# Performance work log

Measured on AMD Instinct MI355X. Metric: run time of the kernel, lower is better.

## Reference

```python
import jax, jax.numpy as jnp
import numpy as np
from jax import lax

L, D, H, F, T = 4, 512, 8, 2048, 1000
B, S = 8, 1024

def setup_inputs() -> dict:
    key = jax.random.key(0)
    ks = jax.random.split(key, 12)
    s = 0.02
    return {
        'features': jax.random.normal(ks[0], (B, S, D), jnp.float32),
        'Wq': jax.random.normal(ks[1], (L, D, D), jnp.float32) * s,
        'Wk': jax.random.normal(ks[2], (L, D, D), jnp.float32) * s,
        'Wv': jax.random.normal(ks[3], (L, D, D), jnp.float32) * s,
        'bq': jnp.zeros((L, D), jnp.float32),
        'bk': jnp.zeros((L, D), jnp.float32),
        'bv': jnp.zeros((L, D), jnp.float32),
        'Wo': jax.random.normal(ks[4], (L, D, D), jnp.float32) * s,
        'bo': jnp.zeros((L, D), jnp.float32),
        'ln1_g': jnp.ones((L, D), jnp.float32),
        'ln1_b': jnp.zeros((L, D), jnp.float32),
        'ln2_g': jnp.ones((L, D), jnp.float32),
        'ln2_b': jnp.zeros((L, D), jnp.float32),
        'W1': jax.random.normal(ks[5], (L, F, D), jnp.float32) * s,
        'b1': jnp.zeros((L, F), jnp.float32),
        'W2': jax.random.normal(ks[6], (L, D, F), jnp.float32) * s,
        'b2': jnp.zeros((L, D), jnp.float32),
        'Wout': jax.random.normal(ks[7], (D, D), jnp.float32) * s,
        'bout': jnp.zeros((D,), jnp.float32),
    }

def _layernorm(x, g, b, eps=1e-5):
    mu = jnp.mean(x, axis=-1, keepdims=True)
    var = jnp.var(x, axis=-1, keepdims=True)
    return (x - mu) / jnp.sqrt(var + eps) * g + b

def _ddim_noise(features):
    betas = jnp.linspace(1e-4, 0.02, T)
    alphas_cumprod = jnp.cumprod(1.0 - betas)
    base = jax.random.key(42)
    def step(x, t):
        a = alphas_cumprod[t]
        noise = jax.random.normal(jax.random.fold_in(base, t), x.shape, x.dtype)
        return jnp.sqrt(a) * x + jnp.sqrt(1.0 - a) * noise, None
    x, _ = lax.scan(step, features, jnp.arange(1, T))
    return x

def reference(features, Wq, Wk, Wv, bq, bk, bv, Wo, bo, ln1_g, ln1_b, ln2_g, ln2_b, W1, b1, W2, b2, Wout, bout):
    x = _ddim_noise(features)  # [B,S,D]
    dh = D // H
    scale = 1.0 / jnp.sqrt(jnp.float32(dh))
    for l in range(L):
        # multi-head self-attention (post-norm, no dropout at eval)
        q = (x @ Wq[l].T + bq[l]).reshape(B, S, H, dh).transpose(0, 2, 1, 3)
        k = (x @ Wk[l].T + bk[l]).reshape(B, S, H, dh).transpose(0, 2, 1, 3)
        v = (x @ Wv[l].T + bv[l]).reshape(B, S, H, dh).transpose(0, 2, 1, 3)
        scores = jnp.einsum('bhqd,bhkd->bhqk', q, k) * scale
        attn = jax.nn.softmax(scores, axis=-1)
        o = jnp.einsum('bhqk,bhkd->bhqd', attn, v).transpose(0, 2, 1, 3).reshape(B, S, D)
        o = o @ Wo[l].T + bo[l]
        x = _layernorm(x + o, ln1_g[l], ln1_b[l])
        # feed-forward (ReLU, PyTorch default)
        ff = jax.nn.relu(x @ W1[l].T + b1[l]) @ W2[l].T + b2[l]
        x = _layernorm(x + ff, ln2_g[l], ln2_b[l])
    return x @ Wout.T + bout
```

## Files before the change

### kernel.cpp

```cpp
#include <hip/hip_runtime.h>
#include <stdint.h>
#include <math.h>

typedef unsigned short u16;
typedef __bf16 bf16x8 __attribute__((ext_vector_type(8)));
typedef float f32x4 __attribute__((ext_vector_type(4)));
typedef short s16x8 __attribute__((ext_vector_type(8)));
union B8 { s16x8 s; bf16x8 b; };

__device__ __forceinline__ u16 f2bf(float f) {
    union { __bf16 h; u16 u; } r;
    r.h = (__bf16)f;
    return r.u;
}
__device__ __forceinline__ uint32_t pk2bf(float a, float b) {
    union { __bf16 h[2]; uint32_t u; } r;
    r.h[0] = (__bf16)a; r.h[1] = (__bf16)b;
    return r.u;
}
__device__ __forceinline__ float bf2f(u16 u) {
    return __uint_as_float(((uint32_t)u) << 16);
}
__device__ __forceinline__ float fexp2(float x) {
    return __builtin_amdgcn_exp2f(x);
}

typedef const __attribute__((address_space(1))) uint32_t* gas_t;
typedef __attribute__((address_space(3))) uint32_t* las_t;
__device__ __forceinline__ void gld16(const void* g, void* l) {
    __builtin_amdgcn_global_load_lds((gas_t)g, (las_t)l, 16, 0, 0);
}

__host__ __forceinline__ uint32_t rotl32(uint32_t x, int d) {
    return (x << d) | (x >> (32 - d));
}
__device__ __forceinline__ uint32_t rotl_d(uint32_t x, int d) {
    return __builtin_amdgcn_alignbit(x, x, (uint32_t)(32 - d));
}

__host__ inline void tf2x32_h(uint32_t k0, uint32_t k1, uint32_t& x0, uint32_t& x1) {
    uint32_t k2 = k0 ^ k1 ^ 0x1BD11BDAu;
    x0 += k0; x1 += k1;
    x0 += x1; x1 = rotl32(x1, 13); x1 ^= x0;
    x0 += x1; x1 = rotl32(x1, 15); x1 ^= x0;
    x0 += x1; x1 = rotl32(x1, 26); x1 ^= x0;
    x0 += x1; x1 = rotl32(x1,  6); x1 ^= x0;
    x0 += k1; x1 += k2 + 1u;
    x0 += x1; x1 = rotl32(x1, 17); x1 ^= x0;
    x0 += x1; x1 = rotl32(x1, 29); x1 ^= x0;
    x0 += x1; x1 = rotl32(x1, 16); x1 ^= x0;
    x0 += x1; x1 = rotl32(x1, 24); x1 ^= x0;
    x0 += k2; x1 += k0 + 2u;
    x0 += x1; x1 = rotl32(x1, 13); x1 ^= x0;
    x0 += x1; x1 = rotl32(x1, 15); x1 ^= x0;
    x0 += x1; x1 = rotl32(x1, 26); x1 ^= x0;
    x0 += x1; x1 = rotl32(x1,  6); x1 ^= x0;
    x0 += k0; x1 += k1 + 3u;
    x0 += x1; x1 = rotl32(x1, 17); x1 ^= x0;
    x0 += x1; x1 = rotl32(x1, 29); x1 ^= x0;
    x0 += x1; x1 = rotl32(x1, 16); x1 ^= x0;
    x0 += x1; x1 = rotl32(x1, 24); x1 ^= x0;
    x0 += k1; x1 += k2 + 4u;
    x0 += x1; x1 = rotl32(x1, 13); x1 ^= x0;
    x0 += x1; x1 = rotl32(x1, 15); x1 ^= x0;
    x0 += x1; x1 = rotl32(x1, 26); x1 ^= x0;
    x0 += x1; x1 = rotl32(x1,  6); x1 ^= x0;
    x0 += k2; x1 += k0 + 5u;
}

__device__ __forceinline__ void tf2x32_d(uint32_t k0, uint32_t k1,
                                         uint32_t& x0, uint32_t& x1) {
    uint32_t k2 = k0 ^ k1 ^ 0x1BD11BDAu;
    x0 += k0; x1 += k1;
    x0 += x1; x1 = rotl_d(x1, 13); x1 ^= x0;
    x0 += x1; x1 = rotl_d(x1, 15); x1 ^= x0;
    x0 += x1; x1 = rotl_d(x1, 26); x1 ^= x0;
    x0 += x1; x1 = rotl_d(x1,  6); x1 ^= x0;
    x0 += k1; x1 += k2 + 1u;
    x0 += x1; x1 = rotl_d(x1, 17); x1 ^= x0;
    x0 += x1; x1 = rotl_d(x1, 29); x1 ^= x0;
    x0 += x1; x1 = rotl_d(x1, 16); x1 ^= x0;
    x0 += x1; x1 = rotl_d(x1, 24); x1 ^= x0;
    x0 += k2; x1 += k0 + 2u;
    x0 += x1; x1 = rotl_d(x1, 13); x1 ^= x0;
    x0 += x1; x1 = rotl_d(x1, 15); x1 ^= x0;
    x0 += x1; x1 = rotl_d(x1, 26); x1 ^= x0;
    x0 += x1; x1 = rotl_d(x1,  6); x1 ^= x0;
    x0 += k0; x1 += k1 + 3u;
    x0 += x1; x1 = rotl_d(x1, 17); x1 ^= x0;
    x0 += x1; x1 = rotl_d(x1, 29); x1 ^= x0;
    x0 += x1; x1 = rotl_d(x1, 16); x1 ^= x0;
    x0 += x1; x1 = rotl_d(x1, 24); x1 ^= x0;
    x0 += k1; x1 += k2 + 4u;
    x0 += x1; x1 = rotl_d(x1, 13); x1 ^= x0;
    x0 += x1; x1 = rotl_d(x1, 15); x1 ^= x0;
    x0 += x1; x1 = rotl_d(x1, 26); x1 ^= x0;
    x0 += x1; x1 = rotl_d(x1,  6); x1 ^= x0;
    x0 += k2; x1 += k0 + 5u;
}

__device__ __forceinline__ float erfinv_f(float x) {
    float w = -__logf(fmaf(x, -x, 1.0f));
    float p;
    if (w < 5.0f) {
        w = w - 2.5f;
        p = 2.81022636e-08f;
        p = p * w + 3.43273939e-07f;
        p = p * w + -3.5233877e-06f;
        p = p * w + -4.39150654e-06f;
        p = p * w + 0.00021858087f;
        p = p * w + -0.00125372503f;
        p = p * w + -0.00417768164f;
        p = p * w + 0.246640727f;
        p = p * w + 1.50140941f;
    } else {
        w = sqrtf(w) - 3.0f;
        p = -0.000200214257f;
        p = p * w + 0.000100950558f;
        p = p * w + 0.00134934322f;
        p = p * w + -0.00367342844f;
        p = p * w + 0.00573950773f;
        p = p * w + -0.0076224613f;
        p = p * w + 0.00943887047f;
        p = p * w + 1.00167406f;
        p = p * w + 2.83297682f;
    }
    return p * x;
}

__device__ __forceinline__ float tf_normal(uint32_t k0, uint32_t k1, uint32_t idx) {
    uint32_t x0 = 0u, x1 = idx;
    tf2x32_d(k0, k1, x0, x1);
    uint32_t bits = x0 ^ x1;
    float f = __uint_as_float((bits >> 9) | 0x3f800000u) - 1.0f;
    float u = f * 2.0f - 0.99999994f;
    u = fmaxf(-0.99999994f, u);
    return 1.41421354f * erfinv_f(u);
}

__global__ __launch_bounds__(256) void noise_kernel(
    u16* __restrict__ xb,
    uint32_t ka0, uint32_t ka1, float ca,
    uint32_t kb0, uint32_t kb1, float cb, int n4)
{
    int i = blockIdx.x * 256 + threadIdx.x;
    if (i >= n4) return;
    ushort4 vb;
    #pragma unroll
    for (int e = 0; e < 4; ++e) {
        uint32_t idx = (uint32_t)(i * 4 + e);
        float a = ca * tf_normal(ka0, ka1, idx)
                + cb * tf_normal(kb0, kb1, idx);
        (&vb.x)[e] = f2bf(a);
    }
    ((ushort4*)xb)[i] = vb;
}

__global__ __launch_bounds__(256) void cvt_all_kernel(
    const float* __restrict__ Wq, const float* __restrict__ Wk,
    const float* __restrict__ Wv, const float* __restrict__ Wo,
    const float* __restrict__ W1, const float* __restrict__ W2,
    const float* __restrict__ Wout, u16* __restrict__ dst, int n4)
{
    int i = blockIdx.x * 256 + threadIdx.x;
    if (i >= n4) return;
    int e = i * 4;
    const float* src;
    if (e < 3145728) {
        int l = e / 786432;
        int rem = e - l * 786432;
        int sel = rem >> 18;
        int off = rem & 262143;
        src = (sel == 0 ? Wq : sel == 1 ? Wk : Wv) + l * 262144 + off;
    } else if (e < 4194304) src = Wo + (e - 3145728);
    else if (e < 8388608)  src = W1 + (e - 4194304);
    else if (e < 12582912) src = W2 + (e - 8388608);
    else                   src = Wout + (e - 12582912);
    float4 v = *(const float4*)src;
    uint2 o;
    o.x = pk2bf(v.x, v.y);
    o.y = pk2bf(v.z, v.w);
    *(uint2*)(dst + e) = o;
}

template<int EPI>
__global__ __launch_bounds__(512) void gemm64u(
    const u16* __restrict__ A, const u16* __restrict__ Bw,
    const float* __restrict__ bias0, const float* __restrict__ bias1,
    const float* __restrict__ bias2, const u16* __restrict__ resid,
    void* __restrict__ out0, void* __restrict__ out1, void* __restrict__ out2,
    int N, int K)
{
    constexpr int ACH = 16;
    constexpr int ASZ = 128 * 64, BSZ = 64 * 64;
    __shared__ __align__(16) u16 At[2 * ASZ];
    __shared__ __align__(16) u16 Bt[2 * BSZ];
    const int tid = threadIdx.x;
    const int l = tid & 63;
    const int w = tid >> 6;
    const int wr = w >> 1, wc = w & 1;

    int lid = blockIdx.y * gridDim.x + blockIdx.x;
    int nwg = gridDim.x * gridDim.y;
    int nlid = (lid & 7) * (nwg >> 3) + (lid >> 3);
    int mb = nlid / gridDim.x;
    int nb = nlid - mb * gridDim.x;

    const int lrow = l >> 3;
    const int lch  = (l & 7) ^ lrow;

    const u16* aTile = A  + (size_t)(mb * 128) * K + (size_t)lrow * K + lch * 8;
    const u16* bTile = Bw + (size_t)(nb * 64) * K + (size_t)lrow * K + lch * 8;

    f32x4 acc[2][2] = {};

    auto stage = [&](int buf, int k0) {
        #pragma unroll
        for (int i = 0; i < 3; ++i) {
            int c = w * 3 + i;
            if (c < ACH) gld16(aTile + (size_t)(c * 8) * K + k0, &At[buf * ASZ + c * 512]);
            else gld16(bTile + (size_t)((c - ACH) * 8) * K + k0, &Bt[buf * BSZ + (c - ACH) * 512]);
        }
    };
    auto compute = [&](int buf) {
        const u16* Ac = &At[buf * ASZ];
        const u16* Bc = &Bt[buf * BSZ];
        #pragma unroll
        for (int kc = 0; kc < 2; ++kc) {
            B8 af[2], bfr[2];
            #pragma unroll
            for (int m = 0; m < 2; ++m) {
                int r = wr * 32 + m * 16 + (l & 15);
                int ch = kc * 4 + (l >> 4);
                af[m].s = *(const s16x8*)&Ac[r * 64 + ((ch ^ (r & 7)) * 8)];
            }
            #pragma unroll
            for (int n = 0; n < 2; ++n) {
                int r = wc * 32 + n * 16 + (l & 15);
                int ch = kc * 4 + (l >> 4);
                bfr[n].s = *(const s16x8*)&Bc[r * 64 + ((ch ^ (r & 7)) * 8)];
            }
            #pragma unroll
            for (int m = 0; m < 2; ++m)
                #pragma unroll
                for (int n = 0; n < 2; ++n)
                    acc[m][n] = __builtin_amdgcn_mfma_f32_16x16x32_bf16(
                        af[m].b, bfr[n].b, acc[m][n], 0, 0, 0);
        }
    };

    stage(0, 0);
    __syncthreads();
    int cur = 0;
    for (int k0 = 0; k0 < K; k0 += 64) {
        if (k0 + 64 < K) stage(cur ^ 1, k0 + 64);
        compute(cur);
        __syncthreads();
        cur ^= 1;
    }

    if constexpr (EPI == 3) {
        int which = nb >> 3;
        int colseg = (nb & 7) * 64 + wc * 32;
        const float* biasp = which == 0 ? bias0 : which == 1 ? bias1 : bias2;
        float bcol[2];
        #pragma unroll
        for (int n = 0; n < 2; ++n)
            bcol[n] = biasp[colseg + n * 16 + (l & 15)];
        if (which == 2) {
            u16* vT = (u16*)out2;
            #pragma unroll
            for (int m = 0; m < 2; ++m) {
                int row0 = mb * 128 + wr * 32 + m * 16 + (l >> 4) * 4;
                int bb = row0 >> 10, s0 = row0 & 1023;
                #pragma unroll
                for (int n = 0; n < 2; ++n) {
                    int col = colseg + n * 16 + (l & 15);
                    int hh = col >> 6, dd = col & 63;
                    uint2 o;
                    o.x = pk2bf(acc[m][n][0] + bcol[n], acc[m][n][1] + bcol[n]);
                    o.y = pk2bf(acc[m][n][2] + bcol[n], acc[m][n][3] + bcol[n]);
                    *(uint2*)&vT[((size_t)((bb * 8 + hh) * 64 + dd)) * 1024 + s0] = o;
                }
            }
            return;
        }
        float oscale = (which == 0) ? 0.18033688f : 1.0f;
        u16* outp = (u16*)(which == 0 ? out0 : out1);
        #pragma unroll
        for (int m = 0; m < 2; ++m) {
            #pragma unroll
            for (int j = 0; j < 4; ++j) {
                int row = mb * 128 + wr * 32 + m * 16 + (l >> 4) * 4 + j;
                #pragma unroll
                for (int n = 0; n < 2; ++n) {
                    int col = colseg + n * 16 + (l & 15);
                    outp[(size_t)row * 512 + col] = f2bf((acc[m][n][j] + bcol[n]) * oscale);
                }
            }
        }
        return;
    }

    float bcol[2];
    #pragma unroll
    for (int n = 0; n < 2; ++n)
        bcol[n] = bias0[nb * 64 + wc * 32 + n * 16 + (l & 15)];

    #pragma unroll
    for (int m = 0; m < 2; ++m) {
        #pragma unroll
        for (int j = 0; j < 4; ++j) {
            int row = mb * 128 + wr * 32 + m * 16 + (l >> 4) * 4 + j;
            #pragma unroll
            for (int n = 0; n < 2; ++n) {
                int col = nb * 64 + wc * 32 + n * 16 + (l & 15);
                float v = acc[m][n][j] + bcol[n];
                if constexpr (EPI == 1) v += bf2f(resid[(size_t)row * N + col]);
                if constexpr (EPI == 2) v = fmaxf(v, 0.0f);
                if constexpr (EPI == 0) ((float*)out0)[(size_t)row * N + col] = v;
                else                    ((u16*)out0)[(size_t)row * N + col] = f2bf(v);
            }
        }
    }
}

__global__ __launch_bounds__(256) void ln_kernel(
    const u16* __restrict__ y, const float* __restrict__ g,
    const float* __restrict__ b, u16* __restrict__ xb)
{
    int row = blockIdx.x * 4 + (threadIdx.x >> 6);
    int l = threadIdx.x & 63;
    uint4 vv = ((const uint4*)(y + (size_t)row * 512))[l];
    uint32_t wsr[4] = {vv.x, vv.y, vv.z, vv.w};
    float xv[8];
    #pragma unroll
    for (int k = 0; k < 4; ++k) {
        xv[2 * k]     = __uint_as_float(wsr[k] << 16);
        xv[2 * k + 1] = __uint_as_float(wsr[k] & 0xFFFF0000u);
    }
    float s = 0.0f, q = 0.0f;
    #pragma unroll
    for (int k = 0; k < 8; ++k) { s += xv[k]; q += xv[k] * xv[k]; }
    #pragma unroll
    for (int m = 1; m < 64; m <<= 1) {
        s += __shfl_xor(s, m, 64);
        q += __shfl_xor(q, m, 64);
    }
    float mean = s * (1.0f / 512.0f);
    float var  = q * (1.0f / 512.0f) - mean * mean;
    float rstd = rsqrtf(var + 1e-5f);
    const float4* gv = (const float4*)g;
    const float4* bv = (const float4*)b;
    float4 g0 = gv[2 * l], g1 = gv[2 * l + 1];
    float4 b0 = bv[2 * l], b1 = bv[2 * l + 1];
    float ov[8];
    ov[0] = (xv[0] - mean) * rstd * g0.x + b0.x;
    ov[1] = (xv[1] - mean) * rstd * g0.y + b0.y;
    ov[2] = (xv[2] - mean) * rstd * g0.z + b0.z;
    ov[3] = (xv[3] - mean) * rstd * g0.w + b0.w;
    ov[4] = (xv[4] - mean) * rstd * g1.x + b1.x;
    ov[5] = (xv[5] - mean) * rstd * g1.y + b1.y;
    ov[6] = (xv[6] - mean) * rstd * g1.z + b1.z;
    ov[7] = (xv[7] - mean) * rstd * g1.w + b1.w;
    uint4 o;
    o.x = pk2bf(ov[0], ov[1]);
    o.y = pk2bf(ov[2], ov[3]);
    o.z = pk2bf(ov[4], ov[5]);
    o.w = pk2bf(ov[6], ov[7]);
    ((uint4*)(xb + (size_t)row * 512))[l] = o;
}

__global__ __launch_bounds__(512) void attn_kernel(
    const u16* __restrict__ Q, const u16* __restrict__ Km,
    const u16* __restrict__ vT, u16* __restrict__ O)
{
    __shared__ __align__(16) u16 Kt[2][64 * 64];
    __shared__ __align__(16) u16 Vt[2][64 * 64];
    __shared__ __align__(16) char Pl[8][4096];
    const int tid = threadIdx.x;
    const int l = tid & 63;
    const int w = tid >> 6;
    const int g = l >> 4;
    const int q15 = l & 15;
    const int bh = blockIdx.x;
    const int qb = blockIdx.y;
    const int b = bh >> 3, h = bh & 7;
    const int rowQ0 = b * 1024 + qb * 256 + w * 32;
    const int colh = h * 64;
    char* pl = &Pl[w][0];

    const int srow = l >> 3;
    const u16* Kbase = Km + (size_t)(b * 1024) * 512 + colh;
    const u16* Vbase = vT + (size_t)bh * 64 * 1024;

    B8 qf[2][2];
    #pragma unroll
    for (int qt = 0; qt < 2; ++qt)
        #pragma unroll
        for (int kc = 0; kc < 2; ++kc)
            qf[qt][kc].s = *(const s16x8*)&Q[(size_t)(rowQ0 + qt * 16 + q15) * 512
                                            + colh + kc * 32 + g * 8];

    f32x4 oacc[4][2] = {};
    float lrun[2] = {0.0f, 0.0f};

    auto stage = [&](int buf, int kt) {
        int r = w * 8 + srow;
        int cc = (l & 7) ^ (r & 7);
        gld16(Kbase + (size_t)(kt * 64 + r) * 512 + cc * 8, &Kt[buf][w * 512]);
        gld16(Vbase + (size_t)r * 1024 + kt * 64 + cc * 8, &Vt[buf][w * 512]);
    };

    stage(0, 0);
    __syncthreads();
    int cur = 0;

    for (int kt = 0; kt < 16; ++kt) {
        if (kt < 15) stage(cur ^ 1, kt + 1);
        const u16* KtL = &Kt[cur][0];
        const u16* VtL = &Vt[cur][0];

        f32x4 st[2][4];
        #pragma unroll
        for (int mt = 0; mt < 4; ++mt) {
            int r = mt * 16 + q15;
            B8 kf0, kf1;
            kf0.s = *(const s16x8*)&KtL[r * 64 + ((g ^ (r & 7)) * 8)];
            kf1.s = *(const s16x8*)&KtL[r * 64 + (((4 + g) ^ (r & 7)) * 8)];
            #pragma unroll
            for (int qt = 0; qt < 2; ++qt) {
                f32x4 t = {0.f, 0.f, 0.f, 0.f};
                t = __builtin_amdgcn_mfma_f32_16x16x32_bf16(kf0.b, qf[qt][0].b, t, 0, 0, 0);
                t = __builtin_amdgcn_mfma_f32_16x16x32_bf16(kf1.b, qf[qt][1].b, t, 0, 0, 0);
                st[qt][mt] = t;
            }
        }

        #pragma unroll
        for (int qt = 0; qt < 2; ++qt) {
            int qrow = qt * 16 + q15;
            int rbase = qrow * 128;
            int sw = (qrow & 7) << 4;
            float rs = 0.0f;
            #pragma unroll
            for (int mt = 0; mt < 4; ++mt) {
                float e0 = fexp2(st[qt][mt][0]);
                float e1 = fexp2(st[qt][mt][1]);
                float e2 = fexp2(st[qt][mt][2]);
                float e3 = fexp2(st[qt][mt][3]);
                rs += (e0 + e1) + (e2 + e3);
                uint2 pk;
                pk.x = pk2bf(e0, e1);
                pk.y = pk2bf(e2, e3);
                *(uint2*)(pl + rbase + ((mt * 32 + g * 8) ^ sw)) = pk;
            }
            rs += __shfl_xor(rs, 16, 64);
            rs += __shfl_xor(rs, 32, 64);
            lrun[qt] += rs;
        }

        B8 pf[2][2];
        #pragma unroll
        for (int qt = 0; qt < 2; ++qt) {
            int qrow = qt * 16 + q15;
            int sw = (qrow & 7) << 4;
            pf[qt][0].s = *(const s16x8*)(pl + qrow * 128 + ((g * 16) ^ sw));
            pf[qt][1].s = *(const s16x8*)(pl + qrow * 128 + (((4 + g) * 16) ^ sw));
        }

        #pragma unroll
        for (int dt = 0; dt < 4; ++dt) {
            int r = dt * 16 + q15;
            B8 vf0, vf1;
            vf0.s = *(const s16x8*)&VtL[r * 64 + ((g ^ (r & 7)) * 8)];
            vf1.s = *(const s16x8*)&VtL[r * 64 + (((4 + g) ^ (r & 7)) * 8)];
            #pragma unroll
            for (int qt = 0; qt < 2; ++qt) {
                oacc[dt][qt] = __builtin_amdgcn_mfma_f32_16x16x32_bf16(
                    vf0.b, pf[qt][0].b, oacc[dt][qt], 0, 0, 0);
                oacc[dt][qt] = __builtin_amdgcn_mfma_f32_16x16x32_bf16(
                    vf1.b, pf[qt][1].b, oacc[dt][qt], 0, 0, 0);
            }
        }
        __syncthreads();
        cur ^= 1;
    }

    #pragma unroll
    for (int qt = 0; qt < 2; ++qt) {
        float inv = 1.0f / lrun[qt];
        int row = rowQ0 + qt * 16 + q15;
        #pragma unroll
        for (int dt = 0; dt < 4; ++dt) {
            uint2 o;
            o.x = pk2bf(oacc[dt][qt][0] * inv, oacc[dt][qt][1] * inv);
            o.y = pk2bf(oacc[dt][qt][2] * inv, oacc[dt][qt][3] * inv);
            *(uint2*)&O[(size_t)row * 512 + colh + dt * 16 + g * 4] = o;
        }
    }
}

extern "C" void kernel_launch(void* const* d_in, const int* in_sizes, int n_in,
                              void* d_out, int out_size, void* d_ws, size_t ws_size,
                              hipStream_t stream)
{
    const int D = 512, F = 2048, Lc = 4;
    const int Mrows = 8 * 1024;

    const float* Wq   = (const float*)d_in[1];
    const float* Wk   = (const float*)d_in[2];
    const float* Wv   = (const float*)d_in[3];
    const float* bq   = (const float*)d_in[4];
    const float* bk   = (const float*)d_in[5];
    const float* bv   = (const float*)d_in[6];
    const float* Wo   = (const float*)d_in[7];
    const float* bo   = (const float*)d_in[8];
    const float* ln1g = (const float*)d_in[9];
    const float* ln1b = (const float*)d_in[10];
    const float* ln2g = (const float*)d_in[11];
    const float* ln2b = (const float*)d_in[12];
    const float* W1   = (const float*)d_in[13];
    const float* b1   = (const float*)d_in[14];
    const float* W2   = (const float*)d_in[15];
    const float* b2   = (const float*)d_in[16];
    const float* Wout = (const float*)d_in[17];
    const float* bout = (const float*)d_in[18];

    char* p = (char*)d_ws;
    auto alloc = [&](size_t bytes) {
        char* r = p;
        p += (bytes + 255) & ~(size_t)255;
        return r;
    };
    u16* xb = (u16*)alloc((size_t)Mrows * D * 2);
    u16* y  = (u16*)alloc((size_t)Mrows * D * 2);
    char* pool = alloc((size_t)Mrows * F * 2);
    u16* qb_ = (u16*)pool;
    u16* kb_ = (u16*)(pool + (size_t)Mrows * D * 2);
    u16* vT  = (u16*)(pool + (size_t)Mrows * D * 2 * 2);
    u16* ao  = (u16*)(pool + (size_t)Mrows * D * 2 * 3);
    u16* ff1 = (u16*)pool;
    u16* wAll  = (u16*)alloc((size_t)12845056 * 2);
    u16* wqkvB = wAll;
    u16* woB   = wAll + 3145728;
    u16* w1B   = wAll + 4194304;
    u16* w2B   = wAll + 8388608;
    u16* woutB = wAll + 12582912;

    {
        int n4 = 12845056 / 4;
        cvt_all_kernel<<<(n4 + 255) / 256, 256, 0, stream>>>(
            Wq, Wk, Wv, Wo, W1, W2, Wout, wAll, n4);
    }

    float ac[1000];
    {
        float start = 1e-4f, stop = 0.02f;
        float delta = (stop - start) / 999.0f;
        float prod = 1.0f;
        for (int i = 0; i < 1000; ++i) {
            float beta = start + (float)i * delta;
            prod *= (1.0f - beta);
            ac[i] = prod;
        }
    }
    int ts[2] = {999, 998};
    double cs[2];
    double tail = 1.0;
    for (int idx = 0; idx < 2; ++idx) {
        int t = ts[idx];
        cs[idx] = sqrt(1.0 - (double)ac[t]) * tail;
        tail *= sqrt((double)ac[t]);
    }
    uint32_t kk[2][2];
    for (int idx = 0; idx < 2; ++idx) {
        uint32_t x0 = 0u, x1 = (uint32_t)ts[idx];
        tf2x32_h(0u, 42u, x0, x1);
        kk[idx][0] = x0; kk[idx][1] = x1;
    }
    int n4tot = Mrows * D / 4;
    noise_kernel<<<(n4tot + 255) / 256, 256, 0, stream>>>(
        xb,
        kk[0][0], kk[0][1], (float)cs[0],
        kk[1][0], kk[1][1], (float)cs[1], n4tot);

    dim3 gqkv(3 * D / 64, Mrows / 128);
    dim3 g64(D / 64, Mrows / 128);
    dim3 gff1(F / 64, Mrows / 128);

    for (int l = 0; l < Lc; ++l) {
        const u16* wqkv_l = wqkvB + (size_t)l * 3 * D * D;
        const u16* wo_l = woB + (size_t)l * D * D;
        const u16* w1_l = w1B + (size_t)l * F * D;
        const u16* w2_l = w2B + (size_t)l * D * F;

        gemm64u<3><<<gqkv, 512, 0, stream>>>(
            xb, wqkv_l, bq + l * D, bk + l * D, bv + l * D, nullptr,
            qb_, kb_, vT, 3 * D, D);
        attn_kernel<<<dim3(64, 4), 512, 0, stream>>>(qb_, kb_, vT, ao);
        gemm64u<1><<<g64, 512, 0, stream>>>(
            ao, wo_l, bo + l * D, nullptr, nullptr, xb,
            y, nullptr, nullptr, D, D);
        ln_kernel<<<Mrows / 4, 256, 0, stream>>>(y, ln1g + l * D, ln1b + l * D, xb);
        gemm64u<2><<<gff1, 512, 0, stream>>>(
            xb, w1_l, b1 + l * F, nullptr, nullptr, nullptr,
            ff1, nullptr, nullptr, F, D);
        gemm64u<1><<<g64, 512, 0, stream>>>(
            ff1, w2_l, b2 + l * D, nullptr, nullptr, xb,
            y, nullptr, nullptr, D, F);
        ln_kernel<<<Mrows / 4, 256, 0, stream>>>(y, ln2g + l * D, ln2b + l * D, xb);
    }
    gemm64u<0><<<g64, 512, 0, stream>>>(
        xb, woutB, bout, nullptr, nullptr, nullptr,
        d_out, nullptr, nullptr, D, D);
}
```

Baseline: 588.1 us.

## Halve attention query tile per wave and double grid; add MFMA priority hints

New measurement: 577.7 us, median of 2. No clear change (-1.8%).

```diff
diff --git a/kernel.cpp b/kernel.cpp
--- a/kernel.cpp
+++ b/kernel.cpp
@@ -377,7 +377,7 @@
 {
     __shared__ __align__(16) u16 Kt[2][64 * 64];
     __shared__ __align__(16) u16 Vt[2][64 * 64];
-    __shared__ __align__(16) char Pl[8][4096];
+    __shared__ __align__(16) char Pl[8][2048];
     const int tid = threadIdx.x;
     const int l = tid & 63;
     const int w = tid >> 6;
@@ -386,24 +386,24 @@
     const int bh = blockIdx.x;
     const int qb = blockIdx.y;
     const int b = bh >> 3, h = bh & 7;
-    const int rowQ0 = b * 1024 + qb * 256 + w * 32;
+    const int rowQ0 = b * 1024 + qb * 128 + w * 16;
     const int colh = h * 64;
     char* pl = &Pl[w][0];
+    const int rbase = q15 * 128;
+    const int sw = (q15 & 7) << 4;
 
     const int srow = l >> 3;
     const u16* Kbase = Km + (size_t)(b * 1024) * 512 + colh;
     const u16* Vbase = vT + (size_t)bh * 64 * 1024;
 
-    B8 qf[2][2];
-    #pragma unroll
-    for (int qt = 0; qt < 2; ++qt)
-        #pragma unroll
-        for (int kc = 0; kc < 2; ++kc)
-            qf[qt][kc].s = *(const s16x8*)&Q[(size_t)(rowQ0 + qt * 16 + q15) * 512
-                                            + colh + kc * 32 + g * 8];
-
-    f32x4 oacc[4][2] = {};
-    float lrun[2] = {0.0f, 0.0f};
+    B8 qf[2];
+    #pragma unroll
+    for (int kc = 0; kc < 2; ++kc)
+        qf[kc].s = *(const s16x8*)&Q[(size_t)(rowQ0 + q15) * 512
+                                     + colh + kc * 32 + g * 8];
+
+    f32x4 oacc[4] = {};
+    float lrun = 0.0f;
 
     auto stage = [&](int buf, int kt) {
         int r = w * 8 + srow;
@@ -421,83 +421,67 @@
         const u16* KtL = &Kt[cur][0];
         const u16* VtL = &Vt[cur][0];
 
-        f32x4 st[2][4];
+        f32x4 st[4];
+        __builtin_amdgcn_s_setprio(1);
         #pragma unroll
         for (int mt = 0; mt < 4; ++mt) {
             int r = mt * 16 + q15;
             B8 kf0, kf1;
             kf0.s = *(const s16x8*)&KtL[r * 64 + ((g ^ (r & 7)) * 8)];
             kf1.s = *(const s16x8*)&KtL[r * 64 + (((4 + g) ^ (r & 7)) * 8)];
-            #pragma unroll
-            for (int qt = 0; qt < 2; ++qt) {
-                f32x4 t = {0.f, 0.f, 0.f, 0.f};
-                t = __builtin_amdgcn_mfma_f32_16x16x32_bf16(kf0.b, qf[qt][0].b, t, 0, 0, 0);
-                t = __builtin_amdgcn_mfma_f32_16x16x32_bf16(kf1.b, qf[qt][1].b, t, 0, 0, 0);
-                st[qt][mt] = t;
-            }
-        }
-
-        #pragma unroll
-        for (int qt = 0; qt < 2; ++qt) {
-            int qrow = qt * 16 + q15;
-            int rbase = qrow * 128;
-            int sw = (qrow & 7) << 4;
-            float rs = 0.0f;
-            #pragma unroll
-            for (int mt = 0; mt < 4; ++mt) {
-                float e0 = fexp2(st[qt][mt][0]);
-                float e1 = fexp2(st[qt][mt][1]);
-                float e2 = fexp2(st[qt][mt][2]);
-                float e3 = fexp2(st[qt][mt][3]);
-                rs += (e0 + e1) + (e2 + e3);
-                uint2 pk;
-                pk.x = pk2bf(e0, e1);
-                pk.y = pk2bf(e2, e3);
-                *(uint2*)(pl + rbase + ((mt * 32 + g * 8) ^ sw)) = pk;
-            }
-            rs += __shfl_xor(rs, 16, 64);
-            rs += __shfl_xor(rs, 32, 64);
-            lrun[qt] += rs;
-        }
-
-        B8 pf[2][2];
-        #pragma unroll
-        for (int qt = 0; qt < 2; ++qt) {
-            int qrow = qt * 16 + q15;
-            int sw = (qrow & 7) << 4;
-            pf[qt][0].s = *(const s16x8*)(pl + qrow * 128 + ((g * 16) ^ sw));
-            pf[qt][1].s = *(const s16x8*)(pl + qrow * 128 + (((4 + g) * 16) ^ sw));
-        }
-
+            f32x4 t = {0.f, 0.f, 0.f, 0.f};
+            t = __builtin_amdgcn_mfma_f32_16x16x32_bf16(kf0.b, qf[0].b, t, 0, 0, 0);
+            t = __builtin_amdgcn_mfma_f32_16x16x32_bf16(kf1.b, qf[1].b, t, 0, 0, 0);
+            st[mt] = t;
+        }
+        __builtin_amdgcn_s_setprio(0);
+
+        float rs = 0.0f;
+        #pragma unroll
+        for (int mt = 0; mt < 4; ++mt) {
+            float e0 = fexp2(st[mt][0]);
+            float e1 = fexp2(st[mt][1]);
+            float e2 = fexp2(st[mt][2]);
+            float e3 = fexp2(st[mt][3]);
+            rs += (e0 + e1) + (e2 + e3);
+            uint2 pk;
+            pk.x = pk2bf(e0, e1);
+            pk.y = pk2bf(e2, e3);
+            *(uint2*)(pl + rbase + ((mt * 32 + g * 8) ^ sw)) = pk;
+        }
+        rs += __shfl_xor(rs, 16, 64);
+        rs += __shfl_xor(rs, 32, 64);
+        lrun += rs;
+
+        B8 pf0, pf1;
+        pf0.s = *(const s16x8*)(pl + rbase + ((g * 16) ^ sw));
+        pf1.s = *(const s16x8*)(pl + rbase + (((4 + g) * 16) ^ sw));
+
+        __builtin_amdgcn_s_setprio(1);
         #pragma unroll
         for (int dt = 0; dt < 4; ++dt) {
             int r = dt * 16 + q15;
             B8 vf0, vf1;
             vf0.s = *(const s16x8*)&VtL[r * 64 + ((g ^ (r & 7)) * 8)];
             vf1.s = *(const s16x8*)&VtL[r * 64 + (((4 + g) ^ (r & 7)) * 8)];
-            #pragma unroll
-            for (int qt = 0; qt < 2; ++qt) {
-                oacc[dt][qt] = __builtin_amdgcn_mfma_f32_16x16x32_bf16(
-                    vf0.b, pf[qt][0].b, oacc[dt][qt], 0, 0, 0);
-                oacc[dt][qt] = __builtin_amdgcn_mfma_f32_16x16x32_bf16(
-                    vf1.b, pf[qt][1].b, oacc[dt][qt], 0, 0, 0);
-            }
-        }
+            oacc[dt] = __builtin_amdgcn_mfma_f32_16x16x32_bf16(
+                vf0.b, pf0.b, oacc[dt], 0, 0, 0);
+            oacc[dt] = __builtin_amdgcn_mfma_f32_16x16x32_bf16(
+                vf1.b, pf1.b, oacc[dt], 0, 0, 0);
+        }
+        __builtin_amdgcn_s_setprio(0);
         __syncthreads();
         cur ^= 1;
     }
 
-    #pragma unroll
-    for (int qt = 0; qt < 2; ++qt) {
-        float inv = 1.0f / lrun[qt];
-        int row = rowQ0 + qt * 16 + q15;
-        #pragma unroll
-        for (int dt = 0; dt < 4; ++dt) {
-            uint2 o;
-            o.x = pk2bf(oacc[dt][qt][0] * inv, oacc[dt][qt][1] * inv);
-            o.y = pk2bf(oacc[dt][qt][2] * inv, oacc[dt][qt][3] * inv);
-            *(uint2*)&O[(size_t)row * 512 + colh + dt * 16 + g * 4] = o;
-        }
+    float inv = 1.0f / lrun;
+    int row = rowQ0 + q15;
+    #pragma unroll
+    for (int dt = 0; dt < 4; ++dt) {
+        uint2 o;
+        o.x = pk2bf(oacc[dt][0] * inv, oacc[dt][1] * inv);
+        o.y = pk2bf(oacc[dt][2] * inv, oacc[dt][3] * inv);
+        *(uint2*)&O[(size_t)row * 512 + colh + dt * 16 + g * 4] = o;
     }
 }
 
@@ -598,7 +582,7 @@
         gemm64u<3><<<gqkv, 512, 0, stream>>>(
             xb, wqkv_l, bq + l * D, bk + l * D, bv + l * D, nullptr,
             qb_, kb_, vT, 3 * D, D);
-        attn_kernel<<<dim3(64, 4), 512, 0, stream>>>(qb_, kb_, vT, ao);
+        attn_kernel<<<dim3(64, 8), 512, 0, stream>>>(qb_, kb_, vT, ao);
         gemm64u<1><<<g64, 512, 0, stream>>>(
             ao, wo_l, bo + l * D, nullptr, nullptr, xb,
             y, nullptr, nullptr, D, D);
```
